# Kernel optimization log

Hardware: AMD Instinct MI355X
Metric: run time of the kernel (lower is better)

Reference implementation:

```python
import jax, jax.numpy as jnp
import numpy as np

N_ENV = 100000   # atomic environments
D = 400          # power-spectrum features
M = 2000         # support points
S = 2000         # structures (row groups)
T = 100          # training slices (column groups)
ZETA = 2


def setup_inputs() -> dict:
    key = jax.random.key(0)
    k1, k2, k3, k4, k5, k6 = jax.random.split(key, 6)
    power_spectrum = jax.random.normal(k1, (N_ENV, D), dtype=jnp.float32)
    sp = jax.random.normal(k2, (M, D), dtype=jnp.float32)
    support_points = sp / jnp.linalg.norm(sp, axis=1, keepdims=True)  # unit-norm, as asserted
    weights = jax.random.normal(k3, (1, T), dtype=jnp.float32)
    all_species = jax.random.randint(k4, (N_ENV,), 0, 5, dtype=jnp.int32)
    row_seg = jnp.sort(jax.random.randint(k5, (N_ENV,), 0, S, dtype=jnp.int32))  # contiguous slices
    col_seg = jnp.sort(jax.random.randint(k6, (M,), 0, T, dtype=jnp.int32))
    return {
        "power_spectrum": power_spectrum,
        "support_points": support_points,
        "weights": weights,
        "all_species": all_species,
        "row_seg": row_seg,
        "col_seg": col_seg,
    }


def reference(power_spectrum, support_points, weights, all_species, row_seg, col_seg):
    # CosineKernel: normalize rows, GEMM against support points, elementwise pow
    ps = power_spectrum / jnp.linalg.norm(power_spectrum, axis=1, keepdims=True)
    k_atom_atom = (ps @ support_points.T) ** ZETA  # [N_ENV, M]
    # SumStructureKernel: block sums over (structure slice, training slice) pairs
    by_struct = jax.ops.segment_sum(k_atom_atom, row_seg, num_segments=S)      # [S, M]
    k = jax.ops.segment_sum(by_struct.T, col_seg, num_segments=T).T            # [S, T]
    return k @ weights.T  # [S, 1]
```

## Files before the change

kernel.cpp:

```cpp
#include <hip/hip_runtime.h>

#define N_ENV 100000
#define DIM   400
#define MPTS  2000
#define NSTR  2000
#define NTRN  100

#define BM 256
#define NPAD 100352
#define KPAD 416
#define MPAD 2048
#define KTILES 13
#define NBLK (NPAD / BM)
#define CSTEPS 32
#define CHUNK 64
#define LDST 424
#define RINGB 53248

typedef __attribute__((ext_vector_type(8))) short short8;
typedef __attribute__((ext_vector_type(4))) short short4v;
typedef __attribute__((ext_vector_type(4))) float float4v;

#define AS1(p) ((const __attribute__((address_space(1))) void*)(p))
#define AS3(p) ((__attribute__((address_space(3))) void*)(p))

__device__ __forceinline__ unsigned short f2bf(float f) {
  union { float f; unsigned int u; } v; v.f = f;
  unsigned int u = v.u;
  u += 0x7fffu + ((u >> 16) & 1u);
  return (unsigned short)(u >> 16);
}
__device__ __forceinline__ float bf2f(unsigned short s) {
  union { unsigned int u; float f; } v; v.u = ((unsigned int)s) << 16;
  return v.f;
}

__global__ __launch_bounds__(256) void prep_kernel(
    const float* __restrict__ w, const int* __restrict__ col_seg,
    float* __restrict__ wm, float* __restrict__ out) {
  int t = blockIdx.x * 256 + threadIdx.x;
  if (t < MPAD) wm[t] = (t < MPTS) ? w[col_seg[t]] : 0.f;
  if (t < NSTR) out[t] = 0.f;
}

__global__ __launch_bounds__(256) void bswz_kernel(
    const float* __restrict__ sp, short8* __restrict__ Bsw) {
  int u = blockIdx.x * 256 + threadIdx.x;
  int lane = u & 63;
  int v = u >> 6;
  int cf = v & 7;
  int w = v >> 3;
  int kt = w % 13;
  int pn = w / 13;
  int col = pn * 128 + cf * 16 + (lane & 15);
  int kb  = kt * 32 + ((lane >> 4) << 3);
  short8 o = (short8){0, 0, 0, 0, 0, 0, 0, 0};
  if (col < MPTS && kb < DIM) {
    const float* p = sp + (size_t)col * DIM + kb;
    float4 a = *(const float4*)p;
    float4 b = *(const float4*)(p + 4);
    o[0] = (short)f2bf(a.x); o[1] = (short)f2bf(a.y);
    o[2] = (short)f2bf(a.z); o[3] = (short)f2bf(a.w);
    o[4] = (short)f2bf(b.x); o[5] = (short)f2bf(b.y);
    o[6] = (short)f2bf(b.z); o[7] = (short)f2bf(b.w);
  }
  Bsw[u] = o;
}

__global__ __launch_bounds__(512, 1) void gemm_fused_kernel(
    const float* __restrict__ A,
    const short8* __restrict__ Bsw,
    const float* __restrict__ wm,
    const int* __restrict__ row_seg,
    float* __restrict__ out) {
  extern __shared__ unsigned char smem[];
  unsigned short* As = (unsigned short*)smem;

  const int tid  = threadIdx.x;
  const int lane = tid & 63;
  const int wid  = tid >> 6;
  const int frow = lane & 15;
  const int koff = (lane >> 4) * 8;
  const long row_base = (long)blockIdx.x * BM;

  short8 af[2][13];

  for (int ch = 0; ch < 4; ++ch) {
    const long rb = row_base + (long)ch * CHUNK;
    int rows_valid = (int)(N_ENV - rb);
    if (rows_valid > CHUNK) rows_valid = CHUNK;
    if (rows_valid < 0) rows_valid = 0;

    {
      const float4v* Ag = (const float4v*)(A + rb * DIM);
      for (int c = tid; c < CHUNK * (DIM / 4); c += 512) {
        int row = c / 100;
        int kc  = c - row * 100;
        uint2 packed = (uint2){0u, 0u};
        if (row < rows_valid) {
          float4v v = __builtin_nontemporal_load(&Ag[c]);
          packed.x = (unsigned int)f2bf(v[0]) | ((unsigned int)f2bf(v[1]) << 16);
          packed.y = (unsigned int)f2bf(v[2]) | ((unsigned int)f2bf(v[3]) << 16);
        }
        *(uint2*)&As[row * LDST + kc * 4] = packed;
      }
      if (tid < CHUNK) {
        uint4 z = (uint4){0u, 0u, 0u, 0u};
        uint4* zp = (uint4*)&As[tid * LDST + 400];
        zp[0] = z; zp[1] = z; zp[2] = z;
      }
    }
    __syncthreads();

    {
      int row = tid >> 3, q = tid & 7;
      unsigned short* rp = &As[row * LDST + q * 52];
      short4v vals[13];
      float ss = 0.f;
#pragma unroll
      for (int i = 0; i < 13; ++i) {
        vals[i] = *(const short4v*)(rp + i * 4);
#pragma unroll
        for (int e = 0; e < 4; ++e) {
          float f = bf2f((unsigned short)vals[i][e]);
          ss += f * f;
        }
      }
      ss += __shfl_xor(ss, 1);
      ss += __shfl_xor(ss, 2);
      ss += __shfl_xor(ss, 4);
      float rn = (ss > 0.f) ? rsqrtf(ss) : 0.f;
#pragma unroll
      for (int i = 0; i < 13; ++i) {
        short4v o;
#pragma unroll
        for (int e = 0; e < 4; ++e)
          o[e] = (short)f2bf(bf2f((unsigned short)vals[i][e]) * rn);
        *(short4v*)(rp + i * 4) = o;
      }
    }
    __syncthreads();

    if ((wid >> 1) == ch) {
      const unsigned short* Ab = &As[((wid & 1) * 32 + frow) * LDST + koff];
#pragma unroll
      for (int i = 0; i < 2; ++i)
#pragma unroll
        for (int kt = 0; kt < 13; ++kt)
          af[i][kt] = *(const short8*)(Ab + i * (16 * LDST) + kt * 32);
    }
    __syncthreads();
  }

  float vacc[2][4];
#pragma unroll
  for (int i = 0; i < 2; ++i)
#pragma unroll
    for (int r = 0; r < 4; ++r) vacc[i][r] = 0.f;

#define STAGE_CSTEP(s)                                                        \
  {                                                                           \
    const int pn_ = (s) >> 1, cfb_ = ((s) & 1) * 4;                           \
    unsigned char* buf_ = smem + (size_t)((s) & 1) * RINGB;                   \
    for (int f = wid; f < 52; f += 8) {                                       \
      int kt_ = f >> 2, j_ = f & 3;                                           \
      const short8* src_ =                                                    \
          Bsw + ((((size_t)pn_ * 13 + kt_) * 8) + cfb_ + j_) * 64 + lane;     \
      __builtin_amdgcn_global_load_lds(AS1(src_), AS3(buf_ + f * 1024),       \
                                       16, 0, 0);                             \
    }                                                                         \
  }

  STAGE_CSTEP(0);
  __syncthreads();

#pragma unroll 1
  for (int s = 0; s < CSTEPS; ++s) {
    if (s + 1 < CSTEPS) STAGE_CSTEP(s + 1);

    const unsigned short* buf =
        (const unsigned short*)(smem + (size_t)(s & 1) * RINGB);

    float wmv[4];
#pragma unroll
    for (int j = 0; j < 4; ++j)
      wmv[j] = wm[s * 64 + j * 16 + frow];

    float4v acc[2][4];
#pragma unroll
    for (int i = 0; i < 2; ++i)
#pragma unroll
      for (int j = 0; j < 4; ++j) acc[i][j] = (float4v){0.f, 0.f, 0.f, 0.f};

    short8 bfc[4], bfn[4];
#pragma unroll
    for (int j = 0; j < 4; ++j)
      bfc[j] = *(const short8*)(buf + j * 512 + lane * 8);

#pragma unroll
    for (int kt = 0; kt < KTILES; ++kt) {
      if (kt + 1 < KTILES) {
#pragma unroll
        for (int j = 0; j < 4; ++j)
          bfn[j] = *(const short8*)(buf + ((kt + 1) * 4 + j) * 512 + lane * 8);
      }
#pragma unroll
      for (int i = 0; i < 2; ++i)
#pragma unroll
        for (int j = 0; j < 4; ++j)
          acc[i][j] = __builtin_amdgcn_mfma_f32_16x16x32_bf16(
              af[i][kt], bfc[j], acc[i][j], 0, 0, 0);
      if (kt + 1 < KTILES) {
#pragma unroll
        for (int j = 0; j < 4; ++j) bfc[j] = bfn[j];
      }
    }

#pragma unroll
    for (int i = 0; i < 2; ++i)
#pragma unroll
      for (int r = 0; r < 4; ++r) {
        float sum = 0.f;
#pragma unroll
        for (int j = 0; j < 4; ++j) {
          float c = acc[i][j][r];
          sum += wmv[j] * c * c;
        }
        vacc[i][r] += sum;
      }

    __syncthreads();
  }

#pragma unroll
  for (int i = 0; i < 2; ++i)
#pragma unroll
    for (int r = 0; r < 4; ++r) {
      float s = vacc[i][r];
      s += __shfl_xor(s, 1);
      s += __shfl_xor(s, 2);
      s += __shfl_xor(s, 4);
      s += __shfl_xor(s, 8);
      if ((lane & 15) == 0) {
        long n = row_base + wid * 32 + i * 16 + (lane >> 4) * 4 + r;
        if (n < N_ENV) atomicAdd(&out[row_seg[n]], s);
      }
    }
}

extern "C" void kernel_launch(void* const* d_in, const int* in_sizes, int n_in,
                              void* d_out, int out_size, void* d_ws, size_t ws_size,
                              hipStream_t stream) {
  const float* ps      = (const float*)d_in[0];
  const float* sp      = (const float*)d_in[1];
  const float* w       = (const float*)d_in[2];
  const int*   row_seg = (const int*)d_in[4];
  const int*   col_seg = (const int*)d_in[5];
  float* out = (float*)d_out;

  char* ws = (char*)d_ws;
  const size_t B_BYTES = (size_t)16 * KTILES * 8 * 64 * 16;
  short8* Bsw = (short8*)ws;
  float*  wm  = (float*)(ws + B_BYTES);

  const int LDS_BYTES = 2 * RINGB;
  (void)hipFuncSetAttribute((const void*)gemm_fused_kernel,
                            hipFuncAttributeMaxDynamicSharedMemorySize,
                            LDS_BYTES);

  prep_kernel<<<MPAD / 256, 256, 0, stream>>>(w, col_seg, wm, out);
  bswz_kernel<<<(16 * KTILES * 8 * 64) / 256, 256, 0, stream>>>(sp, Bsw);
  gemm_fused_kernel<<<NBLK, 512, LDS_BYTES, stream>>>(ps, Bsw, wm, row_seg, out);
}
```

Before: 438.1 us.

## Load B fragments directly from global memory instead of an LDS double buffer

Drops the double-buffered LDS ring that staged pre-swizzled B tiles with global_load_lds, along with the per-step barrier. Each wave now reads its B fragments straight from global memory, relying on L2/MALL to serve the heavily reused 1.6MB B matrix. LDS shrinks to the A staging buffer, which could allow more blocks per CU and removes sync stalls. The cost is higher global load latency inside the MFMA loop, since only a one-step register prefetch hides it.

```diff
diff --git a/kernel.cpp b/kernel.cpp
--- a/kernel.cpp
+++ b/kernel.cpp
@@ -15,14 +15,10 @@
 #define CSTEPS 32
 #define CHUNK 64
 #define LDST 424
-#define RINGB 53248
 
 typedef __attribute__((ext_vector_type(8))) short short8;
 typedef __attribute__((ext_vector_type(4))) short short4v;
 typedef __attribute__((ext_vector_type(4))) float float4v;
-
-#define AS1(p) ((const __attribute__((address_space(1))) void*)(p))
-#define AS3(p) ((__attribute__((address_space(3))) void*)(p))
 
 __device__ __forceinline__ unsigned short f2bf(float f) {
   union { float f; unsigned int u; } v; v.f = f;
@@ -73,8 +69,7 @@
     const float* __restrict__ wm,
     const int* __restrict__ row_seg,
     float* __restrict__ out) {
-  extern __shared__ unsigned char smem[];
-  unsigned short* As = (unsigned short*)smem;
+  __shared__ unsigned short As[CHUNK * LDST];
 
   const int tid  = threadIdx.x;
   const int lane = tid & 63;
@@ -158,28 +153,11 @@
 #pragma unroll
     for (int r = 0; r < 4; ++r) vacc[i][r] = 0.f;
 
-#define STAGE_CSTEP(s)                                                        \
-  {                                                                           \
-    const int pn_ = (s) >> 1, cfb_ = ((s) & 1) * 4;                           \
-    unsigned char* buf_ = smem + (size_t)((s) & 1) * RINGB;                   \
-    for (int f = wid; f < 52; f += 8) {                                       \
-      int kt_ = f >> 2, j_ = f & 3;                                           \
-      const short8* src_ =                                                    \
-          Bsw + ((((size_t)pn_ * 13 + kt_) * 8) + cfb_ + j_) * 64 + lane;     \
-      __builtin_amdgcn_global_load_lds(AS1(src_), AS3(buf_ + f * 1024),       \
-                                       16, 0, 0);                             \
-    }                                                                         \
-  }
-
-  STAGE_CSTEP(0);
-  __syncthreads();
-
 #pragma unroll 1
   for (int s = 0; s < CSTEPS; ++s) {
-    if (s + 1 < CSTEPS) STAGE_CSTEP(s + 1);
-
-    const unsigned short* buf =
-        (const unsigned short*)(smem + (size_t)(s & 1) * RINGB);
+    const int pn  = s >> 1;
+    const int cfb = (s & 1) * 4;
+    const short8* Bc = Bsw + ((size_t)pn * 104 + cfb) * 64 + lane;
 
     float wmv[4];
 #pragma unroll
@@ -194,15 +172,14 @@
 
     short8 bfc[4], bfn[4];
 #pragma unroll
-    for (int j = 0; j < 4; ++j)
-      bfc[j] = *(const short8*)(buf + j * 512 + lane * 8);
+    for (int j = 0; j < 4; ++j) bfc[j] = Bc[(size_t)j * 64];
 
 #pragma unroll
     for (int kt = 0; kt < KTILES; ++kt) {
       if (kt + 1 < KTILES) {
 #pragma unroll
         for (int j = 0; j < 4; ++j)
-          bfn[j] = *(const short8*)(buf + ((kt + 1) * 4 + j) * 512 + lane * 8);
+          bfn[j] = Bc[(size_t)((kt + 1) * 8 + j) * 64];
       }
 #pragma unroll
       for (int i = 0; i < 2; ++i)
@@ -228,8 +205,6 @@
         }
         vacc[i][r] += sum;
       }
-
-    __syncthreads();
   }
 
 #pragma unroll
@@ -263,12 +238,7 @@
   short8* Bsw = (short8*)ws;
   float*  wm  = (float*)(ws + B_BYTES);
 
-  const int LDS_BYTES = 2 * RINGB;
-  (void)hipFuncSetAttribute((const void*)gemm_fused_kernel,
-                            hipFuncAttributeMaxDynamicSharedMemorySize,
-                            LDS_BYTES);
-
   prep_kernel<<<MPAD / 256, 256, 0, stream>>>(w, col_seg, wm, out);
   bswz_kernel<<<(16 * KTILES * 8 * 64) / 256, 256, 0, stream>>>(sp, Bsw);
-  gemm_fused_kernel<<<NBLK, 512, LDS_BYTES, stream>>>(ps, Bsw, wm, row_seg, out);
-}
+  gemm_fused_kernel<<<NBLK, 512, 0, stream>>>(ps, Bsw, wm, row_seg, out);
+}
```

New measurement: 502.4 us. 14.7% more time.
